# Optimization experiments

Hardware: AMD Instinct MI355X
Metric: run time of the kernel (lower is better)

The kernel has to match this reference:

```python
import jax, jax.numpy as jnp
import numpy as np

NUM_CLASSES = 5
TOPK = 10
ALPHA = 0.5
BETA = 6.0
TEMPERATURE = 2.0
EPS = 1e-9
RADIUS = 1.5
MAXF = 5  # max fallback anchors per tiny GT


def setup_inputs() -> dict:
    key = jax.random.key(0)
    ks = jax.random.split(key, 6)
    B, A, G, C = 16, 8400, 128, NUM_CLASSES
    pred_scores = jax.random.normal(ks[0], (B, A, C), jnp.float32)
    pred_bboxes = jax.random.uniform(ks[1], (B, A, 5), jnp.float32)
    anchor_points = jax.random.uniform(ks[2], (A, 2), jnp.float32)
    gt_labels = jax.random.randint(ks[3], (B, G, 1), 0, C, jnp.int32)
    gt_bboxes = jax.random.uniform(ks[4], (B, G, 5), jnp.float32)
    mask_gt = jax.random.randint(ks[5], (B, G, 1), 0, 2, jnp.int32)
    return dict(pred_scores=pred_scores, pred_bboxes=pred_bboxes,
                anchor_points=anchor_points, gt_labels=gt_labels,
                gt_bboxes=gt_bboxes, mask_gt=mask_gt)


def reference(pred_scores, pred_bboxes, anchor_points, gt_labels, gt_bboxes, mask_gt):
    B, A, C = pred_scores.shape
    G = gt_bboxes.shape[1]
    labels = gt_labels[..., 0].astype(jnp.int32)          # [B,G]
    mask = mask_gt[..., 0] > 0                            # [B,G]

    # ---- get_box_metrics ----
    cls_scores = jnp.clip(jax.nn.sigmoid(pred_scores), EPS, 1.0)            # [B,A,C]
    bbox_scores = jnp.take_along_axis(
        cls_scores, jnp.broadcast_to(labels[:, None, :], (B, A, G)), axis=2)  # [B,A,G]
    pred_cxcy = pred_bboxes[:, :, None, :2]                                  # [B,A,1,2]
    gt_cxcy = gt_bboxes[:, None, :, :2]                                      # [B,1,G,2]
    distances = jnp.linalg.norm(pred_cxcy - gt_cxcy, axis=-1)                # [B,A,G]
    gt_wh = gt_bboxes[:, None, :, 2:4]                                       # [B,1,G,2]
    scale = jnp.sqrt(gt_wh[..., 0] * gt_wh[..., 1])                          # [B,1,G]
    overlaps = jnp.exp(-(distances / (scale + 1e-6)) ** 2)                   # [B,A,G]
    align_metric = jnp.exp(ALPHA * jnp.log(bbox_scores + EPS)
                           + BETA * jnp.log(overlaps + EPS))
    ap = anchor_points.reshape(1, A, 1, 2)
    center_dist = jnp.linalg.norm(ap - gt_cxcy, axis=-1)                     # [B,A,G]
    center_weight = jnp.exp(-(center_dist / (scale * 1.5 + 1e-6)) ** 2)
    align_metric = align_metric * center_weight

    # ---- select_candidates_in_gts (rotated boxes) ----
    theta = gt_bboxes[:, None, :, 4]                                         # [B,1,G]
    dx = ap[..., 0] - gt_cxcy[..., 0]
    dy = ap[..., 1] - gt_cxcy[..., 1]
    cos_t, sin_t = jnp.cos(-theta), jnp.sin(-theta)
    local_dx = dx * cos_t - dy * sin_t
    local_dy = dx * sin_t + dy * cos_t
    is_in = ((jnp.abs(local_dx) < gt_wh[..., 0] * RADIUS)
             & (jnp.abs(local_dy) < gt_wh[..., 1] * RADIUS))                 # [B,A,G]

    # ---- tiny-object fallback (unconditional, gated by tiny_missed mask;
    #      equivalent to torch's data-dependent `if` branch) ----
    gt_area = gt_bboxes[..., 2] * gt_bboxes[..., 3]                          # [B,G]
    cand_per_gt = is_in.sum(axis=1)                                          # [B,G]
    tiny_missed = mask & (gt_area < 0.01) & (cand_per_gt == 0)
    fallback_k = jnp.where(gt_area < 0.002, 5, 3)                            # [B,G]
    dist_ga = jnp.linalg.norm(
        gt_bboxes[:, :, None, :2] - anchor_points[None, None, :, :], axis=-1)  # [B,G,A]
    _, closest_idx = jax.lax.top_k(-dist_ga, MAXF)                           # [B,G,5]
    seq = jnp.arange(MAXF)[None, None, :]
    valid_fb = tiny_missed[:, :, None] & (seq < fallback_k[:, :, None])      # [B,G,5]
    b_grid = jnp.arange(B)[:, None, None]
    g_grid = jnp.arange(G)[None, :, None]
    fb = jnp.zeros((B, A, G), jnp.int32).at[b_grid, closest_idx, g_grid].max(
        valid_fb.astype(jnp.int32))
    is_in = is_in | (fb > 0)

    align_metric = align_metric * is_in.astype(align_metric.dtype)

    # ---- select_topk_candidates ----
    am_gT = jnp.swapaxes(align_metric, 1, 2) * mask[:, :, None].astype(align_metric.dtype)  # [B,G,A]
    ov_gT = jnp.swapaxes(overlaps, 1, 2)                                     # [B,G,A]
    topk_metrics, topk_idxs = jax.lax.top_k(am_gT, TOPK)                     # [B,G,K]
    topk_overlaps = jnp.take_along_axis(ov_gT, topk_idxs, axis=2)
    dynamic_k = jnp.clip(jnp.round(topk_overlaps.sum(-1)), 1.0, float(TOPK)) # [B,G]
    k_mask = jnp.arange(TOPK)[None, None, :] < dynamic_k[:, :, None]
    pos_vals = (topk_metrics > EPS) & k_mask
    is_pos_gT = jnp.zeros((B, G, A), bool).at[b_grid, g_grid, topk_idxs].set(pos_vals)

    align_metric = jnp.swapaxes(am_gT, 1, 2)                                 # [B,A,G] (GT-masked)
    is_pos = jnp.swapaxes(is_pos_gT, 1, 2)                                   # [B,A,G]
    anchor_to_gt = jnp.argmax(align_metric, axis=-1)                         # [B,A]
    is_pos_mask = is_pos.sum(-1) > 0                                         # [B,A]
    target_labels = jnp.take_along_axis(labels, anchor_to_gt, axis=1)        # [B,A]
    target_bboxes = jnp.take_along_axis(
        gt_bboxes, jnp.broadcast_to(anchor_to_gt[:, :, None], (B, A, 5)), axis=1)  # [B,A,5]
    am_max = align_metric.max(axis=1, keepdims=True)                         # [B,1,G]
    norm_am = align_metric / (am_max + EPS) * overlaps                       # [B,A,G]
    raw = jnp.take_along_axis(norm_am, anchor_to_gt[:, :, None], axis=2)[..., 0]  # [B,A]
    valid = (target_labels >= 0) & (target_labels < C) & is_pos_mask
    raw_safe = jnp.where(raw > 0, raw, 1.0)
    soft = jnp.where(raw > 0, raw_safe ** (1.0 / TEMPERATURE), 0.0)
    target_scores = jax.nn.one_hot(target_labels, C, dtype=pred_scores.dtype) \
        * (soft * valid.astype(soft.dtype))[..., None]                       # [B,A,C]
    return target_labels, target_bboxes, target_scores, is_pos_mask
```

## Files before the change

kernel.cpp:

```cpp
#include <hip/hip_runtime.h>
#include <math.h>

#define NB 16
#define NA 8400
#define NG 128
#define NC 5
#define KTOP 10
#define MAXF 5

static __device__ __forceinline__ double lgs64_of(float x) {
    double s = 1.0 / (1.0 + exp(-(double)x));
    s = fmin(fmax(s, 1e-9), 1.0);
    return log(s + 1e-9);
}

static __device__ __forceinline__ unsigned fenc(float f) {
    unsigned u = __float_as_uint(f);
    return (u & 0x80000000u) ? ~u : (u | 0x80000000u);
}
static __device__ __forceinline__ float fdec(unsigned e) {
    return (e & 0x80000000u) ? __uint_as_float(e ^ 0x80000000u) : __uint_as_float(~e);
}

static __device__ __forceinline__ void t_bounds(
    float lgsf, float r2, float cr2, float& lb, float& ub)
{
    float A = -r2;
    float Llo = fmaxf(A, -20.723267f);
    float lw = (A > -16.0f || A < -25.0f) ? 0.014f : 0.6932f;
    float base = 0.5f * lgsf + 6.0f * Llo - cr2;
    float mm = 5e-4f + 1e-5f * (fabsf(lgsf) + 6.0f * fabsf(Llo) + cr2);
    lb = base - mm;
    ub = base + 6.0f * lw + mm;
}


__global__ __launch_bounds__(256) void k_prep(
    const float* __restrict__ ps, float* __restrict__ tab, int* __restrict__ pos_mask)
{
    int i = blockIdx.x * 256 + threadIdx.x;
    if (i < NB * NA * NC) {
        float x = ps[i];
        float s = 1.0f / (1.0f + __expf(-x));
        s = fminf(fmaxf(s, 1e-9f), 1.0f);
        tab[i] = __logf(s + 1e-9f);
    }
    if (i < NB * NA) pos_mask[i] = 0;
}


__global__ __launch_bounds__(256) void k_assign(
    const float* __restrict__ pred_scores,
    const float* __restrict__ pred_bboxes,
    const float* __restrict__ anchor_points,
    const int*   __restrict__ gt_labels,
    const float* __restrict__ gt_bboxes,
    const int*   __restrict__ mask_gt,
    const float* __restrict__ lg32,
    int* __restrict__ fb_cnt,
    int* __restrict__ fb_idx,
    double* __restrict__ am_max,
    int* __restrict__ pos_mask)
{
    int bg = blockIdx.x;
    int b = bg / NG;
    int tid = threadIdx.x;
    int lane = tid & 63;
    int wid = tid >> 6;

    const float* gbb = gt_bboxes + (size_t)bg * 5;
    float cxf = gbb[0], cyf = gbb[1];
    double cx = cxf, cy = cyf, w = gbb[2], h = gbb[3], th = gbb[4];
    double ct = cos(-th), st = sin(-th);
    double w15 = w * 1.5, h15 = h * 1.5;
    int m = mask_gt[bg];
    double area = w * h;

    __shared__ float  s_ub[NA];
    __shared__ unsigned s_bar_u;
    __shared__ double LwV[4][KTOP];
    __shared__ int    LwI[4][KTOP];
    __shared__ double wv_s[KTOP];
    __shared__ int    wi_s[KTOP];
    __shared__ int    s_win[MAXF];
    __shared__ int    s_k;
    __shared__ int    s_cnt;

    bool need_fb = (m > 0) && (area < 0.01);
    if (tid == 0) { s_k = 0; s_cnt = 0; s_bar_u = 0u; }
    __syncthreads();

    if (need_fb) {
        int cnt = 0;
        double ld[MAXF]; int lid[MAXF];
#pragma unroll
        for (int t = 0; t < MAXF; t++) { ld[t] = 1e300; lid[t] = 0x7fffffff; }
        for (int a = tid; a < NA; a += 256) {
            float axf = anchor_points[2 * a], ayf = anchor_points[2 * a + 1];
            double cdx = (double)axf - cx, cdy = (double)ayf - cy;
            double ldx = cdx * ct - cdy * st;
            double ldy = cdx * st + cdy * ct;
            if (fabs(ldx) < w15 && fabs(ldy) < h15) cnt++;
            double d = sqrt(cdx * cdx + cdy * cdy);
            double cv = d; int ci = a;
#pragma unroll
            for (int p = 0; p < MAXF; p++) {
                bool better = (cv < ld[p]) || (cv == ld[p] && ci < lid[p]);
                double tv = ld[p]; int ti = lid[p];
                if (better) { ld[p] = cv; lid[p] = ci; cv = tv; ci = ti; }
            }
        }
        for (int off = 32; off; off >>= 1) cnt += __shfl_xor(cnt, off);
        if (lane == 0) atomicAdd(&s_cnt, cnt);
        for (int j = 0; j < MAXF; j++) {
            double bv = ld[0]; int bi = lid[0];
            int hi = lid[0];
            for (int off = 32; off; off >>= 1) {
                double ov = __shfl_xor(bv, off); int oi = __shfl_xor(bi, off);
                if (ov < bv || (ov == bv && oi < bi)) { bv = ov; bi = oi; }
            }
            if (lane == 0) { LwV[wid][j] = bv; LwI[wid][j] = bi; }
            if (hi == bi) {
#pragma unroll
                for (int p = 0; p < MAXF - 1; p++) { ld[p] = ld[p + 1]; lid[p] = lid[p + 1]; }
                ld[MAXF - 1] = 1e301; lid[MAXF - 1] = 0x7fffffff;
            }
        }
        __syncthreads();
        if (tid == 0) {
            int p0 = 0, p1 = 0, p2 = 0, p3 = 0;
            for (int j = 0; j < MAXF; j++) {
                double h0 = (p0 < MAXF) ? LwV[0][p0] : 1e302; int i0 = (p0 < MAXF) ? LwI[0][p0] : 0x7fffffff;
                double h1 = (p1 < MAXF) ? LwV[1][p1] : 1e302; int i1 = (p1 < MAXF) ? LwI[1][p1] : 0x7fffffff;
                double h2 = (p2 < MAXF) ? LwV[2][p2] : 1e302; int i2 = (p2 < MAXF) ? LwI[2][p2] : 0x7fffffff;
                double h3 = (p3 < MAXF) ? LwV[3][p3] : 1e302; int i3 = (p3 < MAXF) ? LwI[3][p3] : 0x7fffffff;
                double bv = h0; int bi = i0; int bw = 0;
                if (h1 < bv || (h1 == bv && i1 < bi)) { bv = h1; bi = i1; bw = 1; }
                if (h2 < bv || (h2 == bv && i2 < bi)) { bv = h2; bi = i2; bw = 2; }
                if (h3 < bv || (h3 == bv && i3 < bi)) { bv = h3; bi = i3; bw = 3; }
                s_win[j] = bi;
                if (bw == 0) p0++; else if (bw == 1) p1++; else if (bw == 2) p2++; else p3++;
            }
            int total = s_cnt;
            int k = 0;
            if (total == 0) k = (area < 0.002) ? 5 : 3;
            s_k = k;
            for (int j = 0; j < MAXF; j++) fb_idx[bg * MAXF + j] = s_win[j];
        }
        __syncthreads();
    }
    if (tid == 0) fb_cnt[bg] = s_k;

    if (m <= 0) {
        if (tid == 0) am_max[bg] = 0.0;
        return;
    }
    __syncthreads();

    double scale = sqrt(w * h);
    float scalef = (float)scale;
    float sef = scalef + 1e-6f;
    float se2f = scalef * 1.5f + 1e-6f;
    float iq1f = 1.0f / (sef * sef);
    float iq2f = 1.0f / (se2f * se2f);
    int lbl = gt_labels[bg];
    int fcnt = s_k;
    int fidx[MAXF];
#pragma unroll
    for (int t = 0; t < MAXF; t++) fidx[t] = need_fb ? s_win[t] : 0x7fffffff;

    unsigned long long inmask = 0ull;
    float lb10[KTOP];
#pragma unroll
    for (int t = 0; t < KTOP; t++) lb10[t] = -3.0e38f;

    {
        int i = 0;
        for (int a = tid; a < NA; a += 256, ++i) {
            float axf = anchor_points[2 * a], ayf = anchor_points[2 * a + 1];
            double cdx = (double)axf - cx, cdy = (double)ayf - cy;
            double ldx = cdx * ct - cdy * st;
            double ldy = cdx * st + cdy * ct;
            bool inb = (fabs(ldx) < w15) && (fabs(ldy) < h15);
            bool fbh = false;
#pragma unroll
            for (int t = 0; t < MAXF; t++) if (t < fcnt && fidx[t] == a) fbh = true;
            float ub = -3.0e38f;
            if (inb || fbh) {
                inmask |= (1ull << i);
                float pxf = pred_bboxes[((size_t)b * NA + a) * 5 + 0];
                float pyf = pred_bboxes[((size_t)b * NA + a) * 5 + 1];
                float lgsf = lg32[((size_t)b * NA + a) * NC + lbl];
                float dxf = pxf - cxf, dyf = pyf - cyf;
                float r2 = (dxf * dxf + dyf * dyf) * iq1f;
                float cdxf = axf - cxf, cdyf = ayf - cyf;
                float cr2 = (cdxf * cdxf + cdyf * cdyf) * iq2f;
                float lb;
                t_bounds(lgsf, r2, cr2, lb, ub);
#pragma unroll
                for (int p = 0; p < KTOP; p++) {
                    bool better = lb > lb10[p];
                    float tv = lb10[p];
                    if (better) { lb10[p] = lb; lb = tv; }
                }
            }
            s_ub[a] = ub;
        }
    }
    {
        float bv = -3.0e38f;
        for (int j = 0; j < KTOP; j++) {
            bv = lb10[0];
            for (int off = 32; off; off >>= 1)
                bv = fmaxf(bv, __shfl_xor(bv, off));
            if (lb10[0] == bv) {
#pragma unroll
                for (int p = 0; p < KTOP - 1; p++) lb10[p] = lb10[p + 1];
                lb10[KTOP - 1] = -3.0e38f;
            }
        }
        if (lane == 0) atomicMax(&s_bar_u, fenc(bv));
    }
    __syncthreads();
    float bar_t = fdec(s_bar_u);
    bool skip_ok = (bar_t > -700.0f);

    double lv[KTOP]; int li[KTOP];
#pragma unroll
    for (int t = 0; t < KTOP; t++) { lv[t] = -1.0; li[t] = 0x7fffffff; }

    {
        int i = 0;
        for (int a = tid; a < NA; a += 256, ++i) {
            bool act = (inmask >> i) & 1ull;
            double amm; bool have = false;
            if (act) {
                if (!skip_ok || s_ub[a] >= bar_t) {
                    float axf = anchor_points[2 * a], ayf = anchor_points[2 * a + 1];
                    float pxf = pred_bboxes[((size_t)b * NA + a) * 5 + 0];
                    float pyf = pred_bboxes[((size_t)b * NA + a) * 5 + 1];
                    double lgs = lgs64_of(pred_scores[((size_t)b * NA + a) * NC + lbl]);
                    double px = (double)pxf, py = (double)pyf;
                    double dx = px - cx, dy = py - cy;
                    double d  = sqrt(dx * dx + dy * dy);
                    double r  = d / (scale + 1e-6);
                    double e1 = exp(-(r * r));
                    double L  = log(e1 + 1e-9);
                    double cdx = (double)axf - cx, cdy = (double)ayf - cy;
                    double cd = sqrt(cdx * cdx + cdy * cdy);
                    double cr = cd / (scale * 1.5 + 1e-6);
                    amm = exp(0.5 * lgs + 6.0 * L - cr * cr);
                    have = true;
                }
            } else if (!skip_ok) {
                amm = 0.0; have = true;
            }
            if (have) {
                double cv = amm; int ci = a;
#pragma unroll
                for (int p = 0; p < KTOP; p++) {
                    bool better = (cv > lv[p]) || (cv == lv[p] && ci < li[p]);
                    double tv = lv[p]; int ti = li[p];
                    if (better) { lv[p] = cv; li[p] = ci; cv = tv; ci = ti; }
                }
            }
        }
    }

    for (int j = 0; j < KTOP; j++) {
        double bv = lv[0]; int bi = li[0];
        int hi = li[0];
        for (int off = 32; off; off >>= 1) {
            double ov = __shfl_xor(bv, off); int oi = __shfl_xor(bi, off);
            if (ov > bv || (ov == bv && oi < bi)) { bv = ov; bi = oi; }
        }
        if (lane == 0) { LwV[wid][j] = bv; LwI[wid][j] = bi; }
        if (hi == bi) {
#pragma unroll
            for (int p = 0; p < KTOP - 1; p++) { lv[p] = lv[p + 1]; li[p] = li[p + 1]; }
            lv[KTOP - 1] = -2.0; li[KTOP - 1] = 0x7fffffff;
        }
    }
    __syncthreads();

    if (tid == 0) {
        int p0 = 0, p1 = 0, p2 = 0, p3 = 0;
        for (int j = 0; j < KTOP; j++) {
            double h0 = (p0 < KTOP) ? LwV[0][p0] : -3.0; int i0 = (p0 < KTOP) ? LwI[0][p0] : 0x7fffffff;
            double h1 = (p1 < KTOP) ? LwV[1][p1] : -3.0; int i1 = (p1 < KTOP) ? LwI[1][p1] : 0x7fffffff;
            double h2 = (p2 < KTOP) ? LwV[2][p2] : -3.0; int i2 = (p2 < KTOP) ? LwI[2][p2] : 0x7fffffff;
            double h3 = (p3 < KTOP) ? LwV[3][p3] : -3.0; int i3 = (p3 < KTOP) ? LwI[3][p3] : 0x7fffffff;
            double bv = h0; int bi = i0; int bw = 0;
            if (h1 > bv || (h1 == bv && i1 < bi)) { bv = h1; bi = i1; bw = 1; }
            if (h2 > bv || (h2 == bv && i2 < bi)) { bv = h2; bi = i2; bw = 2; }
            if (h3 > bv || (h3 == bv && i3 < bi)) { bv = h3; bi = i3; bw = 3; }
            wv_s[j] = bv; wi_s[j] = bi;
            if (bw == 0) p0++; else if (bw == 1) p1++; else if (bw == 2) p2++; else p3++;
        }
        am_max[bg] = wv_s[0];
        double ssum = 0.0;
        for (int j = 0; j < KTOP; j++) {
            int aW = wi_s[j];
            double px = (double)pred_bboxes[((size_t)b * NA + aW) * 5 + 0];
            double py = (double)pred_bboxes[((size_t)b * NA + aW) * 5 + 1];
            double dx = px - cx, dy = py - cy;
            double d = sqrt(dx * dx + dy * dy);
            double r = d / (scale + 1e-6);
            ssum += exp(-(r * r));
        }
        double rk = rint(ssum);
        rk = fmin(fmax(rk, 1.0), 10.0);
        for (int j = 0; j < KTOP; j++) {
            if (wv_s[j] > 1e-9 && (double)j < rk)
                atomicOr(&pos_mask[b * NA + wi_s[j]], 1);
        }
    }
}


__global__ __launch_bounds__(256) void k_final(
    const float* __restrict__ pred_scores,
    const float* __restrict__ pred_bboxes,
    const float* __restrict__ anchor_points,
    const int*   __restrict__ gt_labels,
    const float* __restrict__ gt_bboxes,
    const int*   __restrict__ mask_gt,
    const float* __restrict__ lg32,
    const int*   __restrict__ fb_cnt,
    const int*   __restrict__ fb_idx,
    const double* __restrict__ am_max,
    const int*   __restrict__ pos_mask,
    float* __restrict__ out)
{
    __shared__ double s_cx[NG], s_cy[NG], s_ct[NG], s_st[NG], s_scale[NG], s_w15[NG], s_h15[NG], s_am[NG];
    __shared__ float  f_cx[NG], f_cy[NG], f_iq1[NG], f_iq2[NG];
    __shared__ int s_lbl[NG], s_msk[NG], s_fcnt[NG];
    __shared__ int s_fidx[NG][MAXF];
    __shared__ double mv[4][64];
    __shared__ int    mg[4][64];
    __shared__ double mo[4][64];
    __shared__ float  barr[4][64];

    int b = blockIdx.y;
    int tid = threadIdx.x;
    if (tid < NG) {
        int g = tid, bgi = b * NG + g;
        const float* gbb = gt_bboxes + (size_t)bgi * 5;
        double th = gbb[4];
        double w = gbb[2], h = gbb[3];
        s_cx[g] = gbb[0]; s_cy[g] = gbb[1];
        s_w15[g] = w * 1.5; s_h15[g] = h * 1.5;
        s_ct[g] = cos(-th); s_st[g] = sin(-th);
        double sc = sqrt(w * h);
        s_scale[g] = sc;
        f_cx[g] = gbb[0]; f_cy[g] = gbb[1];
        float scf = (float)sc;
        float sef = scf + 1e-6f, se2f = scf * 1.5f + 1e-6f;
        f_iq1[g] = 1.0f / (sef * sef);
        f_iq2[g] = 1.0f / (se2f * se2f);
        s_am[g] = am_max[bgi];
        s_lbl[g] = gt_labels[bgi];
        s_msk[g] = mask_gt[bgi];
        s_fcnt[g] = fb_cnt[bgi];
        for (int t = 0; t < MAXF; t++) s_fidx[g][t] = fb_idx[bgi * MAXF + t];
    }
    __syncthreads();

    int al = tid & 63;
    int slice = tid >> 6;
    int g0 = slice * 32;
    int a = blockIdx.x * 64 + al;
    bool okA = (a < NA);

    float pxf = 0.f, pyf = 0.f, axf = 0.f, ayf = 0.f;
    float l0 = 0.f, l1 = 0.f, l2 = 0.f, l3 = 0.f, l4 = 0.f;
    unsigned actmask = 0u;
    float bestlb = -3.0e38f;

    if (okA) {
        pxf = pred_bboxes[((size_t)b * NA + a) * 5 + 0];
        pyf = pred_bboxes[((size_t)b * NA + a) * 5 + 1];
        axf = anchor_points[2 * a]; ayf = anchor_points[2 * a + 1];
        const float* lg = lg32 + ((size_t)b * NA + a) * NC;
        l0 = lg[0]; l1 = lg[1]; l2 = lg[2]; l3 = lg[3]; l4 = lg[4];

        for (int k = 0; k < 32; k++) {
            int g = g0 + k;
            double cdx = (double)axf - s_cx[g], cdy = (double)ayf - s_cy[g];
            double ldx = cdx * s_ct[g] - cdy * s_st[g];
            double ldy = cdx * s_st[g] + cdy * s_ct[g];
            bool inb = (fabs(ldx) < s_w15[g]) && (fabs(ldy) < s_h15[g]);
            bool fbh = false;
            int fc = s_fcnt[g];
#pragma unroll
            for (int t = 0; t < MAXF; t++) if (t < fc && s_fidx[g][t] == a) fbh = true;
            if ((inb || fbh) && s_msk[g] > 0) {
                actmask |= (1u << k);
                int lbl = s_lbl[g];
                float lgsf = (lbl == 0) ? l0 : (lbl == 1) ? l1 : (lbl == 2) ? l2 : (lbl == 3) ? l3 : l4;
                float dxf = pxf - f_cx[g], dyf = pyf - f_cy[g];
                float r2 = (dxf * dxf + dyf * dyf) * f_iq1[g];
                float cdxf = axf - f_cx[g], cdyf = ayf - f_cy[g];
                float cr2 = (cdxf * cdxf + cdyf * cdyf) * f_iq2[g];
                float lb, ub;
                t_bounds(lgsf, r2, cr2, lb, ub);
                bestlb = fmaxf(bestlb, lb);
            }
        }
    }
    barr[slice][al] = bestlb;
    __syncthreads();
    float bar_a = fmaxf(fmaxf(barr[0][al], barr[1][al]), fmaxf(barr[2][al], barr[3][al]));
    bool skip_ok = (bar_a > -700.0f);

    double best = 0.0; int bestg = g0; double bov = 0.0;
    if (okA) {
        for (int k = 0; k < 32; k++) {
            if (!((actmask >> k) & 1u)) continue;
            int g = g0 + k;
            if (skip_ok) {
                int lbl = s_lbl[g];
                float lgsf = (lbl == 0) ? l0 : (lbl == 1) ? l1 : (lbl == 2) ? l2 : (lbl == 3) ? l3 : l4;
                float dxf = pxf - f_cx[g], dyf = pyf - f_cy[g];
                float r2 = (dxf * dxf + dyf * dyf) * f_iq1[g];
                float cdxf = axf - f_cx[g], cdyf = ayf - f_cy[g];
                float cr2 = (cdxf * cdxf + cdyf * cdyf) * f_iq2[g];
                float lb, ub;
                t_bounds(lgsf, r2, cr2, lb, ub);
                if (ub < bar_a) continue;
            }
            int lbl = s_lbl[g];
            double lgs = lgs64_of(pred_scores[((size_t)b * NA + a) * NC + lbl]);
            double px = (double)pxf, py = (double)pyf;
            double dx = px - s_cx[g], dy = py - s_cy[g];
            double d = sqrt(dx * dx + dy * dy);
            double r = d / (s_scale[g] + 1e-6);
            double e1 = exp(-(r * r));
            double L = log(e1 + 1e-9);
            double cdx = (double)axf - s_cx[g], cdy = (double)ayf - s_cy[g];
            double cd = sqrt(cdx * cdx + cdy * cdy);
            double cr = cd / (s_scale[g] * 1.5 + 1e-6);
            double amm = exp(0.5 * lgs + 6.0 * L - cr * cr);
            if (amm > best) { best = amm; bestg = g; bov = e1; }
        }
    }

    mv[slice][al] = best; mg[slice][al] = bestg; mo[slice][al] = bov;
    __syncthreads();

    if (tid < 64) {
        int a2 = blockIdx.x * 64 + tid;
        if (a2 < NA) {
            double B = mv[0][tid]; int G = mg[0][tid]; double OV = mo[0][tid];
#pragma unroll
            for (int s = 1; s < 4; s++) {
                if (mv[s][tid] > B) { B = mv[s][tid]; G = mg[s][tid]; OV = mo[s][tid]; }
            }
            int lbl = s_lbl[G];
            bool pos = pos_mask[b * NA + a2] != 0;
            bool valid = (lbl >= 0 && lbl < NC) && pos;
            double raw = B / (s_am[G] + 1e-9) * OV;
            double soft = (raw > 0.0) ? sqrt(raw) : 0.0;

            size_t ba = (size_t)b * NA + a2;
            out[ba] = (float)lbl;
            const float* gb2 = gt_bboxes + ((size_t)b * NG + G) * 5;
            float* ob = out + (size_t)NB * NA + ba * 5;
            ob[0] = gb2[0]; ob[1] = gb2[1]; ob[2] = gb2[2]; ob[3] = gb2[3]; ob[4] = gb2[4];
            float* os = out + (size_t)NB * NA * 6 + ba * 5;
            float sval = valid ? (float)soft : 0.0f;
#pragma unroll
            for (int c = 0; c < NC; c++) os[c] = (c == lbl) ? sval : 0.0f;
            out[(size_t)NB * NA * 11 + ba] = pos ? 1.0f : 0.0f;
        }
    }
}


extern "C" void kernel_launch(void* const* d_in, const int* in_sizes, int n_in,
                              void* d_out, int out_size, void* d_ws, size_t ws_size,
                              hipStream_t stream)
{
    const float* pred_scores   = (const float*)d_in[0];
    const float* pred_bboxes   = (const float*)d_in[1];
    const float* anchor_points = (const float*)d_in[2];
    const int*   gt_labels     = (const int*)d_in[3];
    const float* gt_bboxes     = (const float*)d_in[4];
    const int*   mask_gt       = (const int*)d_in[5];
    float* out = (float*)d_out;

    char* ws = (char*)d_ws;
    size_t off = 0;
    int* pos_mask = (int*)(ws + off);
    off += (size_t)NB * NA * sizeof(int);
    off = (off + 255) & ~(size_t)255;
    double* amax = (double*)(ws + off);
    off += (size_t)NB * NG * sizeof(double);
    off = (off + 255) & ~(size_t)255;
    int* fb_cnt = (int*)(ws + off);
    off += (size_t)NB * NG * sizeof(int);
    off = (off + 255) & ~(size_t)255;
    int* fb_idx = (int*)(ws + off);
    off += (size_t)NB * NG * MAXF * sizeof(int);
    off = (off + 255) & ~(size_t)255;
    float* lg32 = (float*)(ws + off);

    int nls = NB * NA * NC;
    k_prep<<<(nls + 255) / 256, 256, 0, stream>>>(pred_scores, lg32, pos_mask);
    k_assign<<<NB * NG, 256, 0, stream>>>(pred_scores, pred_bboxes, anchor_points, gt_labels,
                                          gt_bboxes, mask_gt, lg32,
                                          fb_cnt, fb_idx, amax, pos_mask);
    k_final<<<dim3((NA + 63) / 64, NB), 256, 0, stream>>>(
        pred_scores, pred_bboxes, anchor_points, gt_labels, gt_bboxes, mask_gt, lg32,
        fb_cnt, fb_idx, amax, pos_mask, out);
}
```

Baseline: 302.3 us.

## Split per-GT assignment across anchor partitions and merge partial top-k results

```diff
diff --git a/kernel.cpp b/kernel.cpp
--- a/kernel.cpp
+++ b/kernel.cpp
@@ -7,6 +7,8 @@
 #define NC 5
 #define KTOP 10
 #define MAXF 5
+#define SPLIT 4
+#define APART (NA / SPLIT)
 
 static __device__ __forceinline__ double lgs64_of(float x) {
     double s = 1.0 / (1.0 + exp(-(double)x));
@@ -49,7 +51,91 @@
 }
 
 
-__global__ __launch_bounds__(256) void k_assign(
+__global__ __launch_bounds__(256) void k_fb_part(
+    const float* __restrict__ anchor_points,
+    const float* __restrict__ gt_bboxes,
+    const int*   __restrict__ mask_gt,
+    double* __restrict__ pfb_d,
+    int*    __restrict__ pfb_i,
+    int*    __restrict__ pcnt)
+{
+    int bid = blockIdx.x;
+    int bg = bid / SPLIT, p = bid % SPLIT;
+    const float* gbb = gt_bboxes + (size_t)bg * 5;
+    double w = gbb[2], h = gbb[3];
+    int m = mask_gt[bg];
+    double area = w * h;
+    if (!(m > 0 && area < 0.01)) return;
+
+    double cx = gbb[0], cy = gbb[1], th = gbb[4];
+    double ct = cos(-th), st = sin(-th);
+    double w15 = w * 1.5, h15 = h * 1.5;
+    int tid = threadIdx.x, lane = tid & 63, wid = tid >> 6;
+    int a0 = p * APART, a1 = a0 + APART;
+
+    __shared__ int    s_cnt;
+    __shared__ double LwV[4][MAXF];
+    __shared__ int    LwI[4][MAXF];
+    if (tid == 0) s_cnt = 0;
+    __syncthreads();
+
+    int cnt = 0;
+    double ld[MAXF]; int lid[MAXF];
+#pragma unroll
+    for (int t = 0; t < MAXF; t++) { ld[t] = 1e300; lid[t] = 0x7fffffff; }
+    for (int a = a0 + tid; a < a1; a += 256) {
+        float axf = anchor_points[2 * a], ayf = anchor_points[2 * a + 1];
+        double cdx = (double)axf - cx, cdy = (double)ayf - cy;
+        double ldx = cdx * ct - cdy * st;
+        double ldy = cdx * st + cdy * ct;
+        if (fabs(ldx) < w15 && fabs(ldy) < h15) cnt++;
+        double d = sqrt(cdx * cdx + cdy * cdy);
+        double cv = d; int ci = a;
+#pragma unroll
+        for (int q = 0; q < MAXF; q++) {
+            bool better = (cv < ld[q]) || (cv == ld[q] && ci < lid[q]);
+            double tv = ld[q]; int ti = lid[q];
+            if (better) { ld[q] = cv; lid[q] = ci; cv = tv; ci = ti; }
+        }
+    }
+    for (int off = 32; off; off >>= 1) cnt += __shfl_xor(cnt, off);
+    if (lane == 0) atomicAdd(&s_cnt, cnt);
+    for (int j = 0; j < MAXF; j++) {
+        double bv = ld[0]; int bi = lid[0];
+        int hi = lid[0];
+        for (int off = 32; off; off >>= 1) {
+            double ov = __shfl_xor(bv, off); int oi = __shfl_xor(bi, off);
+            if (ov < bv || (ov == bv && oi < bi)) { bv = ov; bi = oi; }
+        }
+        if (lane == 0) { LwV[wid][j] = bv; LwI[wid][j] = bi; }
+        if (hi == bi) {
+#pragma unroll
+            for (int q = 0; q < MAXF - 1; q++) { ld[q] = ld[q + 1]; lid[q] = lid[q + 1]; }
+            ld[MAXF - 1] = 1e301; lid[MAXF - 1] = 0x7fffffff;
+        }
+    }
+    __syncthreads();
+    if (tid == 0) {
+        int p0 = 0, p1 = 0, p2 = 0, p3 = 0;
+        for (int j = 0; j < MAXF; j++) {
+            double h0 = (p0 < MAXF) ? LwV[0][p0] : 1e302; int i0 = (p0 < MAXF) ? LwI[0][p0] : 0x7fffffff;
+            double h1 = (p1 < MAXF) ? LwV[1][p1] : 1e302; int i1 = (p1 < MAXF) ? LwI[1][p1] : 0x7fffffff;
+            double h2 = (p2 < MAXF) ? LwV[2][p2] : 1e302; int i2 = (p2 < MAXF) ? LwI[2][p2] : 0x7fffffff;
+            double h3 = (p3 < MAXF) ? LwV[3][p3] : 1e302; int i3 = (p3 < MAXF) ? LwI[3][p3] : 0x7fffffff;
+            double bv = h0; int bi = i0; int bw = 0;
+            if (h1 < bv || (h1 == bv && i1 < bi)) { bv = h1; bi = i1; bw = 1; }
+            if (h2 < bv || (h2 == bv && i2 < bi)) { bv = h2; bi = i2; bw = 2; }
+            if (h3 < bv || (h3 == bv && i3 < bi)) { bv = h3; bi = i3; bw = 3; }
+            pfb_d[(size_t)bid * MAXF + j] = bv;
+            pfb_i[(size_t)bid * MAXF + j] = bi;
+            if (bw == 0) p0++; else if (bw == 1) p1++; else if (bw == 2) p2++; else p3++;
+        }
+        pcnt[bid] = s_cnt;
+    }
+}
+
+
+__global__ __launch_bounds__(256) void k_topk_part(
     const float* __restrict__ pred_scores,
     const float* __restrict__ pred_bboxes,
     const float* __restrict__ anchor_points,
@@ -57,106 +143,74 @@
     const float* __restrict__ gt_bboxes,
     const int*   __restrict__ mask_gt,
     const float* __restrict__ lg32,
+    const double* __restrict__ pfb_d,
+    const int*    __restrict__ pfb_i,
+    const int*    __restrict__ pcnt,
     int* __restrict__ fb_cnt,
     int* __restrict__ fb_idx,
-    double* __restrict__ am_max,
-    int* __restrict__ pos_mask)
+    double* __restrict__ pt_val,
+    int*    __restrict__ pt_idx)
 {
-    int bg = blockIdx.x;
+    int bid = blockIdx.x;
+    int bg = bid / SPLIT, p = bid % SPLIT;
     int b = bg / NG;
-    int tid = threadIdx.x;
-    int lane = tid & 63;
-    int wid = tid >> 6;
+    int tid = threadIdx.x, lane = tid & 63, wid = tid >> 6;
 
     const float* gbb = gt_bboxes + (size_t)bg * 5;
     float cxf = gbb[0], cyf = gbb[1];
     double cx = cxf, cy = cyf, w = gbb[2], h = gbb[3], th = gbb[4];
-    double ct = cos(-th), st = sin(-th);
-    double w15 = w * 1.5, h15 = h * 1.5;
     int m = mask_gt[bg];
     double area = w * h;
-
-    __shared__ float  s_ub[NA];
+    bool need_fb = (m > 0) && (area < 0.01);
+
+    __shared__ int s_win[MAXF];
+    __shared__ int s_k;
     __shared__ unsigned s_bar_u;
+    __shared__ float s_ub[APART];
     __shared__ double LwV[4][KTOP];
     __shared__ int    LwI[4][KTOP];
-    __shared__ double wv_s[KTOP];
-    __shared__ int    wi_s[KTOP];
-    __shared__ int    s_win[MAXF];
-    __shared__ int    s_k;
-    __shared__ int    s_cnt;
-
-    bool need_fb = (m > 0) && (area < 0.01);
-    if (tid == 0) { s_k = 0; s_cnt = 0; s_bar_u = 0u; }
-    __syncthreads();
-
-    if (need_fb) {
-        int cnt = 0;
-        double ld[MAXF]; int lid[MAXF];
-#pragma unroll
-        for (int t = 0; t < MAXF; t++) { ld[t] = 1e300; lid[t] = 0x7fffffff; }
-        for (int a = tid; a < NA; a += 256) {
-            float axf = anchor_points[2 * a], ayf = anchor_points[2 * a + 1];
-            double cdx = (double)axf - cx, cdy = (double)ayf - cy;
-            double ldx = cdx * ct - cdy * st;
-            double ldy = cdx * st + cdy * ct;
-            if (fabs(ldx) < w15 && fabs(ldy) < h15) cnt++;
-            double d = sqrt(cdx * cdx + cdy * cdy);
-            double cv = d; int ci = a;
-#pragma unroll
-            for (int p = 0; p < MAXF; p++) {
-                bool better = (cv < ld[p]) || (cv == ld[p] && ci < lid[p]);
-                double tv = ld[p]; int ti = lid[p];
-                if (better) { ld[p] = cv; lid[p] = ci; cv = tv; ci = ti; }
-            }
-        }
-        for (int off = 32; off; off >>= 1) cnt += __shfl_xor(cnt, off);
-        if (lane == 0) atomicAdd(&s_cnt, cnt);
-        for (int j = 0; j < MAXF; j++) {
-            double bv = ld[0]; int bi = lid[0];
-            int hi = lid[0];
-            for (int off = 32; off; off >>= 1) {
-                double ov = __shfl_xor(bv, off); int oi = __shfl_xor(bi, off);
-                if (ov < bv || (ov == bv && oi < bi)) { bv = ov; bi = oi; }
-            }
-            if (lane == 0) { LwV[wid][j] = bv; LwI[wid][j] = bi; }
-            if (hi == bi) {
-#pragma unroll
-                for (int p = 0; p < MAXF - 1; p++) { ld[p] = ld[p + 1]; lid[p] = lid[p + 1]; }
-                ld[MAXF - 1] = 1e301; lid[MAXF - 1] = 0x7fffffff;
-            }
-        }
-        __syncthreads();
-        if (tid == 0) {
+
+    if (tid == 0) {
+        s_bar_u = 0u;
+        int k = 0;
+        int win0 = 0x7fffffff, win1 = 0x7fffffff, win2 = 0x7fffffff, win3 = 0x7fffffff, win4 = 0x7fffffff;
+        if (need_fb) {
+            int total = 0;
+            for (int q = 0; q < SPLIT; q++) total += pcnt[bg * SPLIT + q];
             int p0 = 0, p1 = 0, p2 = 0, p3 = 0;
             for (int j = 0; j < MAXF; j++) {
-                double h0 = (p0 < MAXF) ? LwV[0][p0] : 1e302; int i0 = (p0 < MAXF) ? LwI[0][p0] : 0x7fffffff;
-                double h1 = (p1 < MAXF) ? LwV[1][p1] : 1e302; int i1 = (p1 < MAXF) ? LwI[1][p1] : 0x7fffffff;
-                double h2 = (p2 < MAXF) ? LwV[2][p2] : 1e302; int i2 = (p2 < MAXF) ? LwI[2][p2] : 0x7fffffff;
-                double h3 = (p3 < MAXF) ? LwV[3][p3] : 1e302; int i3 = (p3 < MAXF) ? LwI[3][p3] : 0x7fffffff;
+                double h0 = (p0 < MAXF) ? pfb_d[(size_t)(bg * SPLIT + 0) * MAXF + p0] : 1e302;
+                int    i0 = (p0 < MAXF) ? pfb_i[(size_t)(bg * SPLIT + 0) * MAXF + p0] : 0x7fffffff;
+                double h1 = (p1 < MAXF) ? pfb_d[(size_t)(bg * SPLIT + 1) * MAXF + p1] : 1e302;
+                int    i1 = (p1 < MAXF) ? pfb_i[(size_t)(bg * SPLIT + 1) * MAXF + p1] : 0x7fffffff;
+                double h2 = (p2 < MAXF) ? pfb_d[(size_t)(bg * SPLIT + 2) * MAXF + p2] : 1e302;
+                int    i2 = (p2 < MAXF) ? pfb_i[(size_t)(bg * SPLIT + 2) * MAXF + p2] : 0x7fffffff;
+                double h3 = (p3 < MAXF) ? pfb_d[(size_t)(bg * SPLIT + 3) * MAXF + p3] : 1e302;
+                int    i3 = (p3 < MAXF) ? pfb_i[(size_t)(bg * SPLIT + 3) * MAXF + p3] : 0x7fffffff;
                 double bv = h0; int bi = i0; int bw = 0;
                 if (h1 < bv || (h1 == bv && i1 < bi)) { bv = h1; bi = i1; bw = 1; }
                 if (h2 < bv || (h2 == bv && i2 < bi)) { bv = h2; bi = i2; bw = 2; }
                 if (h3 < bv || (h3 == bv && i3 < bi)) { bv = h3; bi = i3; bw = 3; }
-                s_win[j] = bi;
+                if (j == 0) win0 = bi; else if (j == 1) win1 = bi; else if (j == 2) win2 = bi;
+                else if (j == 3) win3 = bi; else win4 = bi;
                 if (bw == 0) p0++; else if (bw == 1) p1++; else if (bw == 2) p2++; else p3++;
             }
-            int total = s_cnt;
-            int k = 0;
             if (total == 0) k = (area < 0.002) ? 5 : 3;
-            s_k = k;
-            for (int j = 0; j < MAXF; j++) fb_idx[bg * MAXF + j] = s_win[j];
-        }
-        __syncthreads();
-    }
-    if (tid == 0) fb_cnt[bg] = s_k;
-
-    if (m <= 0) {
-        if (tid == 0) am_max[bg] = 0.0;
-        return;
-    }
-    __syncthreads();
-
+        }
+        s_k = k;
+        s_win[0] = win0; s_win[1] = win1; s_win[2] = win2; s_win[3] = win3; s_win[4] = win4;
+        if (p == 0) {
+            fb_cnt[bg] = k;
+            fb_idx[bg * MAXF + 0] = win0; fb_idx[bg * MAXF + 1] = win1;
+            fb_idx[bg * MAXF + 2] = win2; fb_idx[bg * MAXF + 3] = win3;
+            fb_idx[bg * MAXF + 4] = win4;
+        }
+    }
+    __syncthreads();
+    if (m <= 0) return;
+
+    double ct = cos(-th), st = sin(-th);
+    double w15 = w * 1.5, h15 = h * 1.5;
     double scale = sqrt(w * h);
     float scalef = (float)scale;
     float sef = scalef + 1e-6f;
@@ -167,16 +221,18 @@
     int fcnt = s_k;
     int fidx[MAXF];
 #pragma unroll
-    for (int t = 0; t < MAXF; t++) fidx[t] = need_fb ? s_win[t] : 0x7fffffff;
-
-    unsigned long long inmask = 0ull;
+    for (int t = 0; t < MAXF; t++) fidx[t] = s_win[t];
+
+    int a0 = p * APART, a1 = a0 + APART;
+
+    unsigned inmask = 0u;
     float lb10[KTOP];
 #pragma unroll
     for (int t = 0; t < KTOP; t++) lb10[t] = -3.0e38f;
 
     {
         int i = 0;
-        for (int a = tid; a < NA; a += 256, ++i) {
+        for (int a = a0 + tid; a < a1; a += 256, ++i) {
             float axf = anchor_points[2 * a], ayf = anchor_points[2 * a + 1];
             double cdx = (double)axf - cx, cdy = (double)ayf - cy;
             double ldx = cdx * ct - cdy * st;
@@ -187,7 +243,7 @@
             for (int t = 0; t < MAXF; t++) if (t < fcnt && fidx[t] == a) fbh = true;
             float ub = -3.0e38f;
             if (inb || fbh) {
-                inmask |= (1ull << i);
+                inmask |= (1u << i);
                 float pxf = pred_bboxes[((size_t)b * NA + a) * 5 + 0];
                 float pyf = pred_bboxes[((size_t)b * NA + a) * 5 + 1];
                 float lgsf = lg32[((size_t)b * NA + a) * NC + lbl];
@@ -197,14 +253,16 @@
                 float cr2 = (cdxf * cdxf + cdyf * cdyf) * iq2f;
                 float lb;
                 t_bounds(lgsf, r2, cr2, lb, ub);
-#pragma unroll
-                for (int p = 0; p < KTOP; p++) {
-                    bool better = lb > lb10[p];
-                    float tv = lb10[p];
-                    if (better) { lb10[p] = lb; lb = tv; }
+                if (lb > lb10[KTOP - 1]) {
+#pragma unroll
+                    for (int q = 0; q < KTOP; q++) {
+                        bool better = lb > lb10[q];
+                        float tv = lb10[q];
+                        if (better) { lb10[q] = lb; lb = tv; }
+                    }
                 }
             }
-            s_ub[a] = ub;
+            s_ub[a - a0] = ub;
         }
     }
     {
@@ -215,7 +273,7 @@
                 bv = fmaxf(bv, __shfl_xor(bv, off));
             if (lb10[0] == bv) {
 #pragma unroll
-                for (int p = 0; p < KTOP - 1; p++) lb10[p] = lb10[p + 1];
+                for (int q = 0; q < KTOP - 1; q++) lb10[q] = lb10[q + 1];
                 lb10[KTOP - 1] = -3.0e38f;
             }
         }
@@ -231,11 +289,11 @@
 
     {
         int i = 0;
-        for (int a = tid; a < NA; a += 256, ++i) {
-            bool act = (inmask >> i) & 1ull;
+        for (int a = a0 + tid; a < a1; a += 256, ++i) {
+            bool act = (inmask >> i) & 1u;
             double amm; bool have = false;
             if (act) {
-                if (!skip_ok || s_ub[a] >= bar_t) {
+                if (!skip_ok || s_ub[a - a0] >= bar_t) {
                     float axf = anchor_points[2 * a], ayf = anchor_points[2 * a + 1];
                     float pxf = pred_bboxes[((size_t)b * NA + a) * 5 + 0];
                     float pyf = pred_bboxes[((size_t)b * NA + a) * 5 + 1];
@@ -258,10 +316,10 @@
             if (have) {
                 double cv = amm; int ci = a;
 #pragma unroll
-                for (int p = 0; p < KTOP; p++) {
-                    bool better = (cv > lv[p]) || (cv == lv[p] && ci < li[p]);
-                    double tv = lv[p]; int ti = li[p];
-                    if (better) { lv[p] = cv; li[p] = ci; cv = tv; ci = ti; }
+                for (int q = 0; q < KTOP; q++) {
+                    bool better = (cv > lv[q]) || (cv == lv[q] && ci < li[q]);
+                    double tv = lv[q]; int ti = li[q];
+                    if (better) { lv[q] = cv; li[q] = ci; cv = tv; ci = ti; }
                 }
             }
         }
@@ -277,7 +335,7 @@
         if (lane == 0) { LwV[wid][j] = bv; LwI[wid][j] = bi; }
         if (hi == bi) {
 #pragma unroll
-            for (int p = 0; p < KTOP - 1; p++) { lv[p] = lv[p + 1]; li[p] = li[p + 1]; }
+            for (int q = 0; q < KTOP - 1; q++) { lv[q] = lv[q + 1]; li[q] = li[q + 1]; }
             lv[KTOP - 1] = -2.0; li[KTOP - 1] = 0x7fffffff;
         }
     }
@@ -294,26 +352,77 @@
             if (h1 > bv || (h1 == bv && i1 < bi)) { bv = h1; bi = i1; bw = 1; }
             if (h2 > bv || (h2 == bv && i2 < bi)) { bv = h2; bi = i2; bw = 2; }
             if (h3 > bv || (h3 == bv && i3 < bi)) { bv = h3; bi = i3; bw = 3; }
-            wv_s[j] = bv; wi_s[j] = bi;
+            pt_val[(size_t)bid * KTOP + j] = bv;
+            pt_idx[(size_t)bid * KTOP + j] = bi;
             if (bw == 0) p0++; else if (bw == 1) p1++; else if (bw == 2) p2++; else p3++;
         }
-        am_max[bg] = wv_s[0];
-        double ssum = 0.0;
-        for (int j = 0; j < KTOP; j++) {
-            int aW = wi_s[j];
-            double px = (double)pred_bboxes[((size_t)b * NA + aW) * 5 + 0];
-            double py = (double)pred_bboxes[((size_t)b * NA + aW) * 5 + 1];
-            double dx = px - cx, dy = py - cy;
-            double d = sqrt(dx * dx + dy * dy);
-            double r = d / (scale + 1e-6);
-            ssum += exp(-(r * r));
-        }
-        double rk = rint(ssum);
-        rk = fmin(fmax(rk, 1.0), 10.0);
-        for (int j = 0; j < KTOP; j++) {
-            if (wv_s[j] > 1e-9 && (double)j < rk)
-                atomicOr(&pos_mask[b * NA + wi_s[j]], 1);
-        }
+    }
+}
+
+
+__global__ __launch_bounds__(256) void k_merge(
+    const float* __restrict__ pred_bboxes,
+    const float* __restrict__ gt_bboxes,
+    const int*   __restrict__ mask_gt,
+    const double* __restrict__ pt_val,
+    const int*    __restrict__ pt_idx,
+    double* __restrict__ am_max,
+    int* __restrict__ pos_mask)
+{
+    int gi = blockIdx.x * 256 + threadIdx.x;
+    if (gi >= NB * NG) return;
+    int b = gi / NG;
+    int m = mask_gt[gi];
+    if (m <= 0) { am_max[gi] = 0.0; return; }
+
+    const float* gbb = gt_bboxes + (size_t)gi * 5;
+    double cx = gbb[0], cy = gbb[1];
+    double scale = sqrt((double)gbb[2] * (double)gbb[3]);
+
+    const double* v0 = pt_val + (size_t)(gi * SPLIT + 0) * KTOP;
+    const double* v1 = pt_val + (size_t)(gi * SPLIT + 1) * KTOP;
+    const double* v2 = pt_val + (size_t)(gi * SPLIT + 2) * KTOP;
+    const double* v3 = pt_val + (size_t)(gi * SPLIT + 3) * KTOP;
+    const int* x0 = pt_idx + (size_t)(gi * SPLIT + 0) * KTOP;
+    const int* x1 = pt_idx + (size_t)(gi * SPLIT + 1) * KTOP;
+    const int* x2 = pt_idx + (size_t)(gi * SPLIT + 2) * KTOP;
+    const int* x3 = pt_idx + (size_t)(gi * SPLIT + 3) * KTOP;
+
+    int p0 = 0, p1 = 0, p2 = 0, p3 = 0;
+    double ssum = 0.0;
+    double wv0 = 0.0;
+    double wvj[KTOP]; int wij[KTOP];
+#pragma unroll
+    for (int j = 0; j < KTOP; j++) {
+        double h0 = (p0 < KTOP) ? v0[p0] : -3.0; int i0 = (p0 < KTOP) ? x0[p0] : 0x7fffffff;
+        double h1 = (p1 < KTOP) ? v1[p1] : -3.0; int i1 = (p1 < KTOP) ? x1[p1] : 0x7fffffff;
+        double h2 = (p2 < KTOP) ? v2[p2] : -3.0; int i2 = (p2 < KTOP) ? x2[p2] : 0x7fffffff;
+        double h3 = (p3 < KTOP) ? v3[p3] : -3.0; int i3 = (p3 < KTOP) ? x3[p3] : 0x7fffffff;
+        double bv = h0; int bi = i0; int bw = 0;
+        if (h1 > bv || (h1 == bv && i1 < bi)) { bv = h1; bi = i1; bw = 1; }
+        if (h2 > bv || (h2 == bv && i2 < bi)) { bv = h2; bi = i2; bw = 2; }
+        if (h3 > bv || (h3 == bv && i3 < bi)) { bv = h3; bi = i3; bw = 3; }
+        wvj[j] = bv; wij[j] = bi;
+        if (j == 0) wv0 = bv;
+        if (bw == 0) p0++; else if (bw == 1) p1++; else if (bw == 2) p2++; else p3++;
+    }
+    am_max[gi] = wv0;
+#pragma unroll
+    for (int j = 0; j < KTOP; j++) {
+        int aW = wij[j];
+        double px = (double)pred_bboxes[((size_t)b * NA + aW) * 5 + 0];
+        double py = (double)pred_bboxes[((size_t)b * NA + aW) * 5 + 1];
+        double dx = px - cx, dy = py - cy;
+        double d = sqrt(dx * dx + dy * dy);
+        double r = d / (scale + 1e-6);
+        ssum += exp(-(r * r));
+    }
+    double rk = rint(ssum);
+    rk = fmin(fmax(rk, 1.0), 10.0);
+#pragma unroll
+    for (int j = 0; j < KTOP; j++) {
+        if (wvj[j] > 1e-9 && (double)j < rk)
+            atomicOr(&pos_mask[b * NA + wij[j]], 1);
     }
 }
 
@@ -334,6 +443,7 @@
 {
     __shared__ double s_cx[NG], s_cy[NG], s_ct[NG], s_st[NG], s_scale[NG], s_w15[NG], s_h15[NG], s_am[NG];
     __shared__ float  f_cx[NG], f_cy[NG], f_iq1[NG], f_iq2[NG];
+    __shared__ float  f_ct[NG], f_st[NG], f_w15[NG], f_h15[NG];
     __shared__ int s_lbl[NG], s_msk[NG], s_fcnt[NG];
     __shared__ int s_fidx[NG][MAXF];
     __shared__ double mv[4][64];
@@ -354,6 +464,8 @@
         double sc = sqrt(w * h);
         s_scale[g] = sc;
         f_cx[g] = gbb[0]; f_cy[g] = gbb[1];
+        f_ct[g] = (float)s_ct[g]; f_st[g] = (float)s_st[g];
+        f_w15[g] = (float)s_w15[g]; f_h15[g] = (float)s_h15[g];
         float scf = (float)sc;
         float sef = scf + 1e-6f, se2f = scf * 1.5f + 1e-6f;
         f_iq1[g] = 1.0f / (sef * sef);
@@ -386,10 +498,21 @@
 
         for (int k = 0; k < 32; k++) {
             int g = g0 + k;
-            double cdx = (double)axf - s_cx[g], cdy = (double)ayf - s_cy[g];
-            double ldx = cdx * s_ct[g] - cdy * s_st[g];
-            double ldy = cdx * s_st[g] + cdy * s_ct[g];
-            bool inb = (fabs(ldx) < s_w15[g]) && (fabs(ldy) < s_h15[g]);
+            float cdxf = axf - f_cx[g], cdyf = ayf - f_cy[g];
+            float ldxf = cdxf * f_ct[g] - cdyf * f_st[g];
+            float ldyf = cdxf * f_st[g] + cdyf * f_ct[g];
+            float axl = fabsf(ldxf), ayl = fabsf(ldyf);
+            float eb = 1e-6f * (fabsf(cdxf) + fabsf(cdyf)) + 1e-6f;
+            bool inb;
+            if (fabsf(axl - f_w15[g]) <= eb + 2e-7f * f_w15[g] ||
+                fabsf(ayl - f_h15[g]) <= eb + 2e-7f * f_h15[g]) {
+                double cdx = (double)axf - s_cx[g], cdy = (double)ayf - s_cy[g];
+                double ldx = cdx * s_ct[g] - cdy * s_st[g];
+                double ldy = cdx * s_st[g] + cdy * s_ct[g];
+                inb = (fabs(ldx) < s_w15[g]) && (fabs(ldy) < s_h15[g]);
+            } else {
+                inb = (axl < f_w15[g]) && (ayl < f_h15[g]);
+            }
             bool fbh = false;
             int fc = s_fcnt[g];
 #pragma unroll
@@ -400,7 +523,6 @@
                 float lgsf = (lbl == 0) ? l0 : (lbl == 1) ? l1 : (lbl == 2) ? l2 : (lbl == 3) ? l3 : l4;
                 float dxf = pxf - f_cx[g], dyf = pyf - f_cy[g];
                 float r2 = (dxf * dxf + dyf * dyf) * f_iq1[g];
-                float cdxf = axf - f_cx[g], cdyf = ayf - f_cy[g];
                 float cr2 = (cdxf * cdxf + cdyf * cdyf) * f_iq2[g];
                 float lb, ub;
                 t_bounds(lgsf, r2, cr2, lb, ub);
@@ -504,12 +626,32 @@
     off += (size_t)NB * NG * MAXF * sizeof(int);
     off = (off + 255) & ~(size_t)255;
     float* lg32 = (float*)(ws + off);
+    off += (size_t)NB * NA * NC * sizeof(float);
+    off = (off + 255) & ~(size_t)255;
+    double* pfb_d = (double*)(ws + off);
+    off += (size_t)NB * NG * SPLIT * MAXF * sizeof(double);
+    off = (off + 255) & ~(size_t)255;
+    int* pfb_i = (int*)(ws + off);
+    off += (size_t)NB * NG * SPLIT * MAXF * sizeof(int);
+    off = (off + 255) & ~(size_t)255;
+    int* pcnt = (int*)(ws + off);
+    off += (size_t)NB * NG * SPLIT * sizeof(int);
+    off = (off + 255) & ~(size_t)255;
+    double* pt_val = (double*)(ws + off);
+    off += (size_t)NB * NG * SPLIT * KTOP * sizeof(double);
+    off = (off + 255) & ~(size_t)255;
+    int* pt_idx = (int*)(ws + off);
 
     int nls = NB * NA * NC;
     k_prep<<<(nls + 255) / 256, 256, 0, stream>>>(pred_scores, lg32, pos_mask);
-    k_assign<<<NB * NG, 256, 0, stream>>>(pred_scores, pred_bboxes, anchor_points, gt_labels,
-                                          gt_bboxes, mask_gt, lg32,
-                                          fb_cnt, fb_idx, amax, pos_mask);
+    k_fb_part<<<NB * NG * SPLIT, 256, 0, stream>>>(anchor_points, gt_bboxes, mask_gt,
+                                                   pfb_d, pfb_i, pcnt);
+    k_topk_part<<<NB * NG * SPLIT, 256, 0, stream>>>(pred_scores, pred_bboxes, anchor_points,
+                                                     gt_labels, gt_bboxes, mask_gt, lg32,
+                                                     pfb_d, pfb_i, pcnt, fb_cnt, fb_idx,
+                                                     pt_val, pt_idx);
+    k_merge<<<(NB * NG + 255) / 256, 256, 0, stream>>>(pred_bboxes, gt_bboxes, mask_gt,
+                                                       pt_val, pt_idx, amax, pos_mask);
     k_final<<<dim3((NA + 63) / 64, NB), 256, 0, stream>>>(
         pred_scores, pred_bboxes, anchor_points, gt_labels, gt_bboxes, mask_gt, lg32,
         fb_cnt, fb_idx, amax, pos_mask, out);
```

Result: slower. 345.8 us (+14.4%).
